# Kernel optimization log

Measured on AMD Instinct MI355X. Metric: run time of the kernel, lower is better.

## Reference

```python
import jax, jax.numpy as jnp
import numpy as np

XY = 16   # xy_size
Z = 16    # z_size
S = XY * XY * Z   # num_states = 4096
V = 2048  # num_tokens


def _build_structure():
    # Static 3D-grid neighbor structure (replaces the per-state Python loop).
    h = np.arange(S)
    zc, rem = np.divmod(h, XY * XY)
    yc, xc = np.divmod(rem, XY)
    coords = np.stack([xc, yc, zc], 1)                       # [S,3] (x,y,z)
    offs = np.array([[0, 0, 0], [1, 0, 0], [-1, 0, 0], [0, 1, 0],
                     [0, -1, 0], [0, 0, 1], [0, 0, 2]])       # 7 fixed offsets
    nc = coords[:, None, :] + offs[None]                      # [S,7,3]
    valid = ((nc[..., 0] >= 0) & (nc[..., 0] < XY) &
             (nc[..., 1] >= 0) & (nc[..., 1] < XY) &
             (nc[..., 2] >= 0) & (nc[..., 2] < Z))
    dest = nc[..., 0] + XY * (nc[..., 1] + XY * nc[..., 2])   # flat neighbor idx
    # compact valid neighbors to the front, preserving offset order:
    # j-th valid neighbor consumes logit j (matches logits[h, :len(valid)])
    order = np.argsort(~valid, axis=1, kind='stable')
    tgt = np.take_along_axis(dest, order, axis=1)
    vmask = np.take_along_axis(valid, order, axis=1)
    tgt = np.where(vmask, tgt, S)  # invalid slots -> dummy column S
    return jnp.asarray(tgt), jnp.asarray(vmask)

TGT, VMASK = _build_structure()


def transition_log_p(trans_w):
    # masked log-softmax over the first k valid logits of each row
    logits = jnp.where(VMASK, trans_w, -1e30)
    logp = jax.nn.log_softmax(logits, axis=1)
    logp = jnp.where(VMASK, logp, -jnp.inf)
    T = jnp.full((S, S + 1), -jnp.inf, trans_w.dtype)
    T = T.at[jnp.arange(S)[:, None], TGT].set(logp)
    return T[:, :S]  # [S,S], row h = log p(transition targets of h)


def smoothed_emission(emis_w):
    em = jax.nn.log_softmax(emis_w, axis=-1).reshape(Z, XY, XY, V)
    lv, rv = em[:, :, :1], em[:, :, -1:]
    lh, rh = em[:, :1], em[:, -1:]
    c = jnp.zeros((Z, 1, 1, V), em.dtype)  # log(1)=0 pad, as in the original
    c2 = lambda *a: jnp.concatenate(a, axis=2)
    c1 = lambda *a: jnp.concatenate(a, axis=1)
    up = c1(c2(lv, em, rv), c2(c, rh, c), c2(c, rh, c))
    dn = c1(c2(c, lh, c), c2(c, lh, c), c2(lv, em, rv))
    lf = c1(c2(lh, c, c), c2(em, rv, rv), c2(rh, c, c))
    rt = c1(c2(c, c, lh), c2(lv, lv, em), c2(c, c, rh))
    cr = c1(c2(c, lh, c), c2(lv, em, rv), c2(c, rh, c))
    mean = jax.nn.logsumexp(jnp.stack((up, dn, lf, rt, cr)), axis=0) - jnp.log(5.0)
    return mean[:, 1:-1, 1:-1].reshape(S, V)


def _forward(stories, trans_w, emis_w, prior_w):
    priors = jax.nn.log_softmax(prior_w)                      # [S]
    em = smoothed_emission(emis_w)                            # [S,V]
    padded = jnp.concatenate([em, jnp.zeros((S, 1), em.dtype)], axis=1)  # [S,V+1]
    # per-(story, step) emission log-prob: sum over sentence tokens
    all_emis = padded.T[stories].sum(axis=2)                  # [B,L,S]
    all_emis = jnp.transpose(all_emis, (1, 0, 2))             # [L,B,S]
    T = transition_log_p(trans_w)                             # [S,S]
    amax = jnp.max(T, axis=1, keepdims=True)                  # [S,1], finite (self-loop)
    P = jnp.exp(T - amax)                                     # [S,S]
    score0 = all_emis[0] + priors                             # [B,S]

    def step(score, em_t):
        # new[b,a] = em_t[b,a] + logsumexp_h(T[a,h] + score[b,h])  (stable log-matmul)
        smax = jnp.max(score, axis=1, keepdims=True)          # [B,1]
        new = em_t + jnp.log(jnp.exp(score - smax) @ P.T) + smax + amax.T
        return new, new

    _, rest = jax.lax.scan(step, score0, all_emis[1:])
    return jnp.concatenate([score0[None], rest], axis=0)      # [L,B,S]


def setup_inputs() -> dict:
    key = jax.random.key(0)
    k1, k2, k3, k4 = jax.random.split(key, 4)
    B, L, W = 8, 32, 8
    return {
        "stories_tensor": jax.random.randint(k1, (B, L, W), 0, V + 1, dtype=jnp.int32),
        "story_length": L,
        "trans_w": jax.random.normal(k2, (S, 7), jnp.float32),
        "emis_w": jax.random.normal(k3, (S, V), jnp.float32),
        "prior_w": jax.random.normal(k4, (S,), jnp.float32),
    }


def reference(stories_tensor, story_length, trans_w, emis_w, prior_w):
    assert stories_tensor.shape[1] == story_length
    return _forward(stories_tensor, trans_w, emis_w, prior_w)
```

## Files before the change

kernel.cpp:

```cpp
#include <hip/hip_runtime.h>
#include <math.h>

#define XYD 16
#define ZD 16
#define SS 4096
#define VV 2048
#define BB 8
#define LL 32
#define WW 8
#define VC 32
#define SM_STRIDE 257

#define GUARD_L 16
#define GUARD_R 512
#define EBUF_N (GUARD_L + SS + GUARD_R)

__device__ __forceinline__ float b2f(unsigned short u) {
    union { unsigned int i; float f; } x; x.i = ((unsigned int)u) << 16; return x.f;
}
__device__ __forceinline__ unsigned short f2b(float f) {
    union { float f; unsigned int i; } x; x.f = f; return (unsigned short)(x.i >> 16);
}

__global__ void k_logZ(const float* __restrict__ emis_w, float* __restrict__ logZ) {
    int wave = threadIdx.x >> 6;
    int lane = threadIdx.x & 63;
    int row  = blockIdx.x * 4 + wave;
    const float* r = emis_w + (size_t)row * VV;
    float vals[32];
    float m = -INFINITY;
#pragma unroll
    for (int k = 0; k < 8; k++) {
        float4 f = ((const float4*)r)[k * 64 + lane];
        vals[k*4+0] = f.x; vals[k*4+1] = f.y; vals[k*4+2] = f.z; vals[k*4+3] = f.w;
    }
#pragma unroll
    for (int k = 0; k < 32; k++) m = fmaxf(m, vals[k]);
#pragma unroll
    for (int o = 32; o; o >>= 1) m = fmaxf(m, __shfl_xor(m, o));
    float sum = 0.f;
#pragma unroll
    for (int k = 0; k < 32; k++) sum += __expf(vals[k] - m);
#pragma unroll
    for (int o = 32; o; o >>= 1) sum += __shfl_xor(sum, o);
    if (lane == 0) logZ[row] = m + __logf(sum);
}

__global__ void k_smooth(const float* __restrict__ emis_w, const float* __restrict__ logZ,
                         float* __restrict__ smT) {
    __shared__ float tileT[VC * SM_STRIDE];
    int z  = blockIdx.x;
    int v0 = blockIdx.y * VC;
    int tid = threadIdx.x;
    int rsub = tid >> 3;
    int c0   = (tid & 7) * 4;

#pragma unroll
    for (int it = 0; it < 8; it++) {
        int r  = it * 32 + rsub;
        int sg = z * 256 + r;
        float lz = logZ[sg];
        float4 w = *(const float4*)(emis_w + (size_t)sg * VV + v0 + c0);
        tileT[(c0+0)*SM_STRIDE + r] = __expf(w.x - lz);
        tileT[(c0+1)*SM_STRIDE + r] = __expf(w.y - lz);
        tileT[(c0+2)*SM_STRIDE + r] = __expf(w.z - lz);
        tileT[(c0+3)*SM_STRIDE + r] = __expf(w.w - lz);
    }
    __syncthreads();

    int x = tid & 15, y = tid >> 4;
    int sxp = (x < 15) ? tid + 1  : tid;
    int sxm = (x > 0)  ? tid - 1  : tid;
    int syp = (y < 15) ? tid + 16 : tid;
    int sym = (y > 0)  ? tid - 16 : tid;
    float* o = smT + (size_t)v0 * SS + z * 256 + tid;
#pragma unroll
    for (int i = 0; i < VC; i++) {
        const float* tb = tileT + i * SM_STRIDE;
        float s = tb[tid] + tb[sxp] + tb[sxm] + tb[syp] + tb[sym];
        o[(size_t)i * SS] = __logf(s * 0.2f);
    }
}

__global__ void k_emis(const int* __restrict__ stories, const float* __restrict__ smT,
                       float* __restrict__ all_emis) {
    int blk = blockIdx.x;
    int t = blk >> 3, b = blk & 7;
    int tid = threadIdx.x;
    int tok[WW];
#pragma unroll
    for (int w = 0; w < WW; w++) tok[w] = stories[(b * LL + t) * WW + w];
#pragma unroll
    for (int i = 0; i < 4; i++) {
        int s = i * 1024 + tid * 4;
        float4 acc = {0.f, 0.f, 0.f, 0.f};
#pragma unroll
        for (int w = 0; w < WW; w++) {
            if (tok[w] < VV) {
                float4 f = *(const float4*)(smT + (size_t)tok[w] * SS + s);
                acc.x += f.x; acc.y += f.y; acc.z += f.z; acc.w += f.w;
            }
        }
        *(float4*)(all_emis + ((size_t)t * BB + b) * SS + s) = acc;
    }
}

__global__ void __launch_bounds__(1024) k_forward(
    const float* __restrict__ trans_w, const float* __restrict__ prior_w,
    const float* __restrict__ all_emis, float* __restrict__ out) {
    __shared__ __align__(16) unsigned short Ebuf[2][EBUF_N];
    __shared__ float red2[2];
    __shared__ float pr[16];
    int b = blockIdx.x;
    int tid = threadIdx.x;
    int lane = tid & 63, wid = tid >> 6;

    if (tid < GUARD_L) { Ebuf[0][tid] = 0; Ebuf[1][tid] = 0; }
    if (tid < GUARD_R) {
        Ebuf[0][GUARD_L + SS + tid] = 0;
        Ebuf[1][GUARD_L + SS + tid] = 0;
    }

    float pw[28], am[4];
    {
        float w7[28];
        const float4* t4 = (const float4*)(trans_w + (size_t)tid * 28);
#pragma unroll
        for (int k = 0; k < 7; k++) ((float4*)w7)[k] = t4[k];
#pragma unroll
        for (int i = 0; i < 4; i++) {
            int j = tid * 4 + i;
            int xx = j & 15, yy = (j >> 4) & 15, zz = j >> 8;
            bool val[7];
            val[0] = true;
            val[1] = (xx < 15); val[2] = (xx > 0);
            val[3] = (yy < 15); val[4] = (yy > 0);
            val[5] = (zz < 15); val[6] = (zz < 14);
            const float* rw = w7 + i * 7;
            float w[7]; int cnt = 0; float m = -INFINITY;
#pragma unroll
            for (int d = 0; d < 7; d++) { if (val[d]) { w[d] = rw[cnt++]; m = fmaxf(m, w[d]); } }
            float se = 0.f;
#pragma unroll
            for (int d = 0; d < 7; d++) if (val[d]) se += __expf(w[d] - m);
#pragma unroll
            for (int d = 0; d < 7; d++) pw[i*7+d] = val[d] ? __expf(w[d] - m) : 0.f;
            am[i] = -__logf(se);
        }
    }

    float4 pv = ((const float4*)prior_w)[tid];
    float4 em = ((const float4*)(all_emis + (size_t)b * SS))[tid];

    float lm = fmaxf(fmaxf(pv.x, pv.y), fmaxf(pv.z, pv.w));
#pragma unroll
    for (int o = 32; o; o >>= 1) lm = fmaxf(lm, __shfl_xor(lm, o));
    if (lane == 0) pr[wid] = lm;
    __syncthreads();
    float gm = pr[0];
#pragma unroll
    for (int w = 1; w < 16; w++) gm = fmaxf(gm, pr[w]);
    __syncthreads();
    float ls = __expf(pv.x - gm) + __expf(pv.y - gm) + __expf(pv.z - gm) + __expf(pv.w - gm);
#pragma unroll
    for (int o = 32; o; o >>= 1) ls += __shfl_xor(ls, o);
    if (lane == 0) pr[wid] = ls;
    __syncthreads();
    float gs = 0.f;
#pragma unroll
    for (int w = 0; w < 16; w++) gs += pr[w];
    float logZp = gm + __logf(gs);

    float v0 = em.x + pv.x - logZp;
    float v1 = em.y + pv.y - logZp;
    float v2 = em.z + pv.z - logZp;
    float v3 = em.w + pv.w - logZp;
    { float4 ov = {v0, v1, v2, v3}; ((float4*)(out + (size_t)b * SS))[tid] = ov; }
    if (tid == 0) red2[0] = v0;
    __syncthreads();
    float g1 = red2[0];
    float XpPrev = g1;
    {
        ushort4 E;
        E.x = f2b(__expf(v0 - XpPrev)); E.y = f2b(__expf(v1 - XpPrev));
        E.z = f2b(__expf(v2 - XpPrev)); E.w = f2b(__expf(v3 - XpPrev));
        *(ushort4*)(&Ebuf[0][GUARD_L + 4 * tid]) = E;
    }
    float Erx = __expf(v0 - XpPrev), Ery = __expf(v1 - XpPrev);
    float Erz = __expf(v2 - XpPrev), Erw = __expf(v3 - XpPrev);

    float4 em_next = ((const float4*)(all_emis + (size_t)BB * SS + (size_t)b * SS))[tid];

    int cur = 0;
    for (int t = 1; t < LL; t++) {
        __syncthreads();
        em = em_next;
        if (t < LL - 1)
            em_next = ((const float4*)(all_emis + ((size_t)(t + 1) * BB + b) * SS))[tid];

        float g0 = red2[cur];
        float Xp = 2.f * g0 - g1;

        const unsigned short* Eb = Ebuf[cur] + GUARD_L + 4 * tid;
        ushort4 YpU = *(const ushort4*)(Eb + 16);
        ushort4 YmU = *(const ushort4*)(Eb - 16);
        ushort4 ZpU = *(const ushort4*)(Eb + 256);
        ushort4 ZqU = *(const ushort4*)(Eb + 512);
        float bx  = b2f(Eb[4]);
        float cxw = b2f(Eb[-1]);

        float a0 = Erx*pw[0]  + Ery*pw[1]  + cxw*pw[2]        + b2f(YpU.x)*pw[3]  + b2f(YmU.x)*pw[4]  + b2f(ZpU.x)*pw[5]  + b2f(ZqU.x)*pw[6];
        float a1 = Ery*pw[7]  + Erz*pw[8]  + Erx*pw[9]        + b2f(YpU.y)*pw[10] + b2f(YmU.y)*pw[11] + b2f(ZpU.y)*pw[12] + b2f(ZqU.y)*pw[13];
        float a2 = Erz*pw[14] + Erw*pw[15] + Ery*pw[16]       + b2f(YpU.z)*pw[17] + b2f(YmU.z)*pw[18] + b2f(ZpU.z)*pw[19] + b2f(ZqU.z)*pw[20];
        float a3 = Erw*pw[21] + bx*pw[22]  + Erz*pw[23]       + b2f(YpU.w)*pw[24] + b2f(YmU.w)*pw[25] + b2f(ZpU.w)*pw[26] + b2f(ZqU.w)*pw[27];

        v0 = em.x + __logf(a0) + XpPrev + am[0];
        v1 = em.y + __logf(a1) + XpPrev + am[1];
        v2 = em.z + __logf(a2) + XpPrev + am[2];
        v3 = em.w + __logf(a3) + XpPrev + am[3];

        { float4 ov = {v0, v1, v2, v3};
          ((float4*)(out + ((size_t)t * BB + b) * SS))[tid] = ov; }

        Erx = __expf(v0 - Xp); Ery = __expf(v1 - Xp);
        Erz = __expf(v2 - Xp); Erw = __expf(v3 - Xp);
        {
            ushort4 E;
            E.x = f2b(Erx); E.y = f2b(Ery); E.z = f2b(Erz); E.w = f2b(Erw);
            *(ushort4*)(&Ebuf[cur ^ 1][GUARD_L + 4 * tid]) = E;
        }
        if (tid == 0) red2[cur ^ 1] = v0;

        g1 = g0; XpPrev = Xp; cur ^= 1;
    }
}

extern "C" void kernel_launch(void* const* d_in, const int* in_sizes, int n_in,
                              void* d_out, int out_size, void* d_ws, size_t ws_size,
                              hipStream_t stream) {
    const int*   stories = (const int*)d_in[0];
    const float* trans_w = (const float*)d_in[2];
    const float* emis_w  = (const float*)d_in[3];
    const float* prior_w = (const float*)d_in[4];
    float* out = (float*)d_out;

    char* ws = (char*)d_ws;
    float* smT      = (float*)(ws);
    float* all_emis = (float*)(ws + (size_t)VV * SS * 4);
    float* logZ     = (float*)(ws + (size_t)VV * SS * 4 + (size_t)LL * BB * SS * 4);

    k_logZ<<<SS / 4, 256, 0, stream>>>(emis_w, logZ);
    k_smooth<<<dim3(ZD, VV / VC), 256, 0, stream>>>(emis_w, logZ, smT);
    k_emis<<<LL * BB, 256, 0, stream>>>(stories, smT, all_emis);
    k_forward<<<BB, 1024, 0, stream>>>(trans_w, prior_w, all_emis, out);
}
```

Baseline: 156.6 us.

## Fuse smoothing and emission gather via token hit lists and atomic scatter

Drops the full smoothed-emission table (V x S floats) written to global memory. Each smoothing block now builds a list of story tokens that fall in its vocabulary chunk and atomically adds its smoothed log values straight into the per-timestep emission buffer, which the logZ kernel zero-fills beforehand. This removes one kernel launch and a large global write/read round trip, at the cost of float atomics, whose accumulation order is nondeterministic, and a hit list capped at 256 entries. The forward kernel also defers each output store by one step so it sits after the barrier and overlaps with the recurrence.

```diff
diff --git a/kernel.cpp b/kernel.cpp
--- a/kernel.cpp
+++ b/kernel.cpp
@@ -10,6 +10,8 @@
 #define WW 8
 #define VC 32
 #define SM_STRIDE 257
+#define NE (BB * LL * WW)
+#define HL 256
 
 #define GUARD_L 16
 #define GUARD_R 512
@@ -22,7 +24,11 @@
     union { float f; unsigned int i; } x; x.f = f; return (unsigned short)(x.i >> 16);
 }
 
-__global__ void k_logZ(const float* __restrict__ emis_w, float* __restrict__ logZ) {
+__global__ void k_logZ(const float* __restrict__ emis_w, float* __restrict__ logZ,
+                       float4* __restrict__ all_emis4) {
+    float4 z4 = {0.f, 0.f, 0.f, 0.f};
+    all_emis4[blockIdx.x * 256 + threadIdx.x] = z4;
+
     int wave = threadIdx.x >> 6;
     int lane = threadIdx.x & 63;
     int row  = blockIdx.x * 4 + wave;
@@ -46,15 +52,24 @@
     if (lane == 0) logZ[row] = m + __logf(sum);
 }
 
-__global__ void k_smooth(const float* __restrict__ emis_w, const float* __restrict__ logZ,
-                         float* __restrict__ smT) {
+__global__ void __launch_bounds__(256) k_smooth_emis(
+    const float* __restrict__ emis_w, const float* __restrict__ logZ,
+    const int* __restrict__ stories, float* __restrict__ all_emis) {
     __shared__ float tileT[VC * SM_STRIDE];
+    __shared__ float smtile[VC * SM_STRIDE];
+    __shared__ int   toks[NE];
+    __shared__ int   hitlist[HL];
+    __shared__ int   nhits;
     int z  = blockIdx.x;
     int v0 = blockIdx.y * VC;
     int tid = threadIdx.x;
+
+    if (tid == 0) nhits = 0;
+#pragma unroll
+    for (int i = 0; i < NE / 256; i++) toks[i * 256 + tid] = stories[i * 256 + tid];
+
     int rsub = tid >> 3;
     int c0   = (tid & 7) * 4;
-
 #pragma unroll
     for (int it = 0; it < 8; it++) {
         int r  = it * 32 + rsub;
@@ -68,40 +83,35 @@
     }
     __syncthreads();
 
+    for (int e = tid; e < NE; e += 256) {
+        unsigned d = (unsigned)(toks[e] - v0);
+        if (d < VC) {
+            int k = atomicAdd(&nhits, 1);
+            if (k < HL) hitlist[k] = e;
+        }
+    }
+
     int x = tid & 15, y = tid >> 4;
     int sxp = (x < 15) ? tid + 1  : tid;
     int sxm = (x > 0)  ? tid - 1  : tid;
     int syp = (y < 15) ? tid + 16 : tid;
     int sym = (y > 0)  ? tid - 16 : tid;
-    float* o = smT + (size_t)v0 * SS + z * 256 + tid;
 #pragma unroll
     for (int i = 0; i < VC; i++) {
         const float* tb = tileT + i * SM_STRIDE;
         float s = tb[tid] + tb[sxp] + tb[sxm] + tb[syp] + tb[sym];
-        o[(size_t)i * SS] = __logf(s * 0.2f);
-    }
-}
-
-__global__ void k_emis(const int* __restrict__ stories, const float* __restrict__ smT,
-                       float* __restrict__ all_emis) {
-    int blk = blockIdx.x;
-    int t = blk >> 3, b = blk & 7;
-    int tid = threadIdx.x;
-    int tok[WW];
-#pragma unroll
-    for (int w = 0; w < WW; w++) tok[w] = stories[(b * LL + t) * WW + w];
-#pragma unroll
-    for (int i = 0; i < 4; i++) {
-        int s = i * 1024 + tid * 4;
-        float4 acc = {0.f, 0.f, 0.f, 0.f};
-#pragma unroll
-        for (int w = 0; w < WW; w++) {
-            if (tok[w] < VV) {
-                float4 f = *(const float4*)(smT + (size_t)tok[w] * SS + s);
-                acc.x += f.x; acc.y += f.y; acc.z += f.z; acc.w += f.w;
-            }
-        }
-        *(float4*)(all_emis + ((size_t)t * BB + b) * SS + s) = acc;
+        smtile[i * SM_STRIDE + tid] = __logf(s * 0.2f);
+    }
+    __syncthreads();
+
+    int nh = nhits; if (nh > HL) nh = HL;
+    float* dst0 = all_emis + z * 256 + tid;
+    for (int h = 0; h < nh; h++) {
+        int e = hitlist[h];
+        int tok = toks[e] - v0;
+        int bb  = e / (LL * WW);
+        int tt  = (e / WW) % LL;
+        atomicAdd(dst0 + ((size_t)tt * BB + bb) * SS, smtile[tok * SM_STRIDE + tid]);
     }
 }
 
@@ -150,7 +160,8 @@
     }
 
     float4 pv = ((const float4*)prior_w)[tid];
-    float4 em = ((const float4*)(all_emis + (size_t)b * SS))[tid];
+    const float4* emp = (const float4*)(all_emis + (size_t)b * SS) + tid;
+    float4 em = *emp;
 
     float lm = fmaxf(fmaxf(pv.x, pv.y), fmaxf(pv.z, pv.w));
 #pragma unroll
@@ -175,28 +186,32 @@
     float v1 = em.y + pv.y - logZp;
     float v2 = em.z + pv.z - logZp;
     float v3 = em.w + pv.w - logZp;
-    { float4 ov = {v0, v1, v2, v3}; ((float4*)(out + (size_t)b * SS))[tid] = ov; }
+    float4 ov_prev = {v0, v1, v2, v3};
+    float4* outp = (float4*)(out + (size_t)b * SS) + tid;
+
     if (tid == 0) red2[0] = v0;
     __syncthreads();
     float g1 = red2[0];
     float XpPrev = g1;
+    float Erx = __expf(v0 - XpPrev), Ery = __expf(v1 - XpPrev);
+    float Erz = __expf(v2 - XpPrev), Erw = __expf(v3 - XpPrev);
     {
         ushort4 E;
-        E.x = f2b(__expf(v0 - XpPrev)); E.y = f2b(__expf(v1 - XpPrev));
-        E.z = f2b(__expf(v2 - XpPrev)); E.w = f2b(__expf(v3 - XpPrev));
+        E.x = f2b(Erx); E.y = f2b(Ery); E.z = f2b(Erz); E.w = f2b(Erw);
         *(ushort4*)(&Ebuf[0][GUARD_L + 4 * tid]) = E;
     }
-    float Erx = __expf(v0 - XpPrev), Ery = __expf(v1 - XpPrev);
-    float Erz = __expf(v2 - XpPrev), Erw = __expf(v3 - XpPrev);
-
-    float4 em_next = ((const float4*)(all_emis + (size_t)BB * SS + (size_t)b * SS))[tid];
+
+    emp += (BB * SS) / 4;
+    float4 em_next = *emp;
 
     int cur = 0;
     for (int t = 1; t < LL; t++) {
         __syncthreads();
+        *outp = ov_prev;
+        outp += (BB * SS) / 4;
+
         em = em_next;
-        if (t < LL - 1)
-            em_next = ((const float4*)(all_emis + ((size_t)(t + 1) * BB + b) * SS))[tid];
+        if (t < LL - 1) { emp += (BB * SS) / 4; em_next = *emp; }
 
         float g0 = red2[cur];
         float Xp = 2.f * g0 - g1;
@@ -209,18 +224,16 @@
         float bx  = b2f(Eb[4]);
         float cxw = b2f(Eb[-1]);
 
-        float a0 = Erx*pw[0]  + Ery*pw[1]  + cxw*pw[2]        + b2f(YpU.x)*pw[3]  + b2f(YmU.x)*pw[4]  + b2f(ZpU.x)*pw[5]  + b2f(ZqU.x)*pw[6];
-        float a1 = Ery*pw[7]  + Erz*pw[8]  + Erx*pw[9]        + b2f(YpU.y)*pw[10] + b2f(YmU.y)*pw[11] + b2f(ZpU.y)*pw[12] + b2f(ZqU.y)*pw[13];
-        float a2 = Erz*pw[14] + Erw*pw[15] + Ery*pw[16]       + b2f(YpU.z)*pw[17] + b2f(YmU.z)*pw[18] + b2f(ZpU.z)*pw[19] + b2f(ZqU.z)*pw[20];
-        float a3 = Erw*pw[21] + bx*pw[22]  + Erz*pw[23]       + b2f(YpU.w)*pw[24] + b2f(YmU.w)*pw[25] + b2f(ZpU.w)*pw[26] + b2f(ZqU.w)*pw[27];
+        float a0 = Erx*pw[0]  + Ery*pw[1]  + cxw*pw[2]  + b2f(YpU.x)*pw[3]  + b2f(YmU.x)*pw[4]  + b2f(ZpU.x)*pw[5]  + b2f(ZqU.x)*pw[6];
+        float a1 = Ery*pw[7]  + Erz*pw[8]  + Erx*pw[9]  + b2f(YpU.y)*pw[10] + b2f(YmU.y)*pw[11] + b2f(ZpU.y)*pw[12] + b2f(ZqU.y)*pw[13];
+        float a2 = Erz*pw[14] + Erw*pw[15] + Ery*pw[16] + b2f(YpU.z)*pw[17] + b2f(YmU.z)*pw[18] + b2f(ZpU.z)*pw[19] + b2f(ZqU.z)*pw[20];
+        float a3 = Erw*pw[21] + bx*pw[22]  + Erz*pw[23] + b2f(YpU.w)*pw[24] + b2f(YmU.w)*pw[25] + b2f(ZpU.w)*pw[26] + b2f(ZqU.w)*pw[27];
 
         v0 = em.x + __logf(a0) + XpPrev + am[0];
         v1 = em.y + __logf(a1) + XpPrev + am[1];
         v2 = em.z + __logf(a2) + XpPrev + am[2];
         v3 = em.w + __logf(a3) + XpPrev + am[3];
-
-        { float4 ov = {v0, v1, v2, v3};
-          ((float4*)(out + ((size_t)t * BB + b) * SS))[tid] = ov; }
+        ov_prev.x = v0; ov_prev.y = v1; ov_prev.z = v2; ov_prev.w = v3;
 
         Erx = __expf(v0 - Xp); Ery = __expf(v1 - Xp);
         Erz = __expf(v2 - Xp); Erw = __expf(v3 - Xp);
@@ -233,6 +246,7 @@
 
         g1 = g0; XpPrev = Xp; cur ^= 1;
     }
+    *outp = ov_prev;
 }
 
 extern "C" void kernel_launch(void* const* d_in, const int* in_sizes, int n_in,
@@ -245,12 +259,10 @@
     float* out = (float*)d_out;
 
     char* ws = (char*)d_ws;
-    float* smT      = (float*)(ws);
-    float* all_emis = (float*)(ws + (size_t)VV * SS * 4);
-    float* logZ     = (float*)(ws + (size_t)VV * SS * 4 + (size_t)LL * BB * SS * 4);
-
-    k_logZ<<<SS / 4, 256, 0, stream>>>(emis_w, logZ);
-    k_smooth<<<dim3(ZD, VV / VC), 256, 0, stream>>>(emis_w, logZ, smT);
-    k_emis<<<LL * BB, 256, 0, stream>>>(stories, smT, all_emis);
+    float* all_emis = (float*)(ws);
+    float* logZ     = (float*)(ws + (size_t)LL * BB * SS * 4);
+
+    k_logZ<<<SS / 4, 256, 0, stream>>>(emis_w, logZ, (float4*)all_emis);
+    k_smooth_emis<<<dim3(ZD, VV / VC), 256, 0, stream>>>(emis_w, logZ, stories, all_emis);
     k_forward<<<BB, 1024, 0, stream>>>(trans_w, prior_w, all_emis, out);
 }
```

Measured after the change: 167.4 us. 6.9% more time.
